# Kernel optimization log

Hardware: AMD Instinct MI355X
Metric: run time of the kernel (lower is better)

## Reference

```python
import jax, jax.numpy as jnp
import numpy as np

INPUT_DIM = 512
OUTPUT_DIM = 256
FAST_ITERATIONS = 100
BATCH = 65536


def setup_inputs() -> dict:
    key = jax.random.key(0)
    kx, kw, km = jax.random.split(key, 3)
    x = jax.random.normal(kx, (BATCH, INPUT_DIM), dtype=jnp.float32)
    # Xavier-uniform init for W [output_dim, input_dim]
    limit = np.sqrt(6.0 / (INPUT_DIM + OUTPUT_DIM))
    W = jax.random.uniform(kw, (OUTPUT_DIM, INPUT_DIM), dtype=jnp.float32,
                           minval=-limit, maxval=limit)
    # M is zeros in the module; use a small random M (spectral radius ~0.5)
    # so the 100-step recurrence is non-trivial but convergent.
    M = jax.random.normal(km, (OUTPUT_DIM, OUTPUT_DIM), dtype=jnp.float32) * (0.5 / np.sqrt(OUTPUT_DIM))
    return {"x": x, "W": W, "M": M}


def reference(x, W, M):
    Wx = x @ W.T  # [B, out]

    def step(y, _):
        return Wx - y @ M, None

    y, _ = jax.lax.scan(step, Wx, None, length=FAST_ITERATIONS)
    return y
```

## Files before the change

kernel.cpp:

```cpp
#include <hip/hip_runtime.h>
#include <hip/hip_bf16.h>


typedef float f32x4 __attribute__((ext_vector_type(4)));
typedef __bf16 bf16x8 __attribute__((ext_vector_type(8)));

#define IN 512
#define OUT 256
#define BATCH 65536

#define GLOAD_LDS16(gp, lp)                                                              \
    __builtin_amdgcn_global_load_lds((const __attribute__((address_space(1))) void*)(gp), \
                                     (__attribute__((address_space(3))) void*)(lp), 16, 0, 0)

__device__ __forceinline__ void chain_core(const float (*sA)[256], const float* __restrict__ B,
                                           int j, int q, float acc[8]) {
#pragma unroll
    for (int r = 0; r < 8; ++r) acc[r] = 0.f;
    const int kbase = q * 64;
#pragma unroll
    for (int it = 0; it < 16; ++it) {
        const int k = kbase + it * 4;
        const float b0 = B[(k + 0) * 256 + j];
        const float b1 = B[(k + 1) * 256 + j];
        const float b2 = B[(k + 2) * 256 + j];
        const float b3 = B[(k + 3) * 256 + j];
#pragma unroll
        for (int r = 0; r < 8; ++r) {
            const f32x4 av = *(const f32x4*)&sA[r][k];
            acc[r] += av[0] * b0 + av[1] * b1 + av[2] * b2 + av[3] * b3;
        }
    }
}

__global__ __launch_bounds__(1024) void nsm_chain_step(const float* __restrict__ Bmat,
                                                       const float* __restrict__ Pin,
                                                       float* __restrict__ Tout,
                                                       float* __restrict__ Pout,
                                                       const int first) {
    __shared__ float sA[8][256];
    __shared__ float ws[4][8][256];
    const int t = threadIdx.x, j = t & 255, q = t >> 8, b = blockIdx.x;
    float acc[8];
    const bool isT = (b < 32);
    if (isT) {
        const int i0 = b * 8;
        sA[2 * q][j]     = Bmat[(i0 + 2 * q) * 256 + j];
        sA[2 * q + 1][j] = Bmat[(i0 + 2 * q + 1) * 256 + j];
    } else {
        const int i0 = (b - 32) * 8;
        if (first) {
            sA[2 * q][j]     = Pin[j * IN + i0 + 2 * q];
            sA[2 * q + 1][j] = Pin[j * IN + i0 + 2 * q + 1];
        } else {
            sA[2 * q][j]     = Pin[(i0 + 2 * q) * 256 + j];
            sA[2 * q + 1][j] = Pin[(i0 + 2 * q + 1) * 256 + j];
        }
    }
    __syncthreads();
    chain_core(sA, Bmat, j, q, acc);
#pragma unroll
    for (int r = 0; r < 8; ++r) ws[q][r][j] = acc[r];
    __syncthreads();
#pragma unroll
    for (int d = 0; d < 2; ++d) {
        const int r = 2 * q + d;
        const float v = ws[0][r][j] + ws[1][r][j] + ws[2][r][j] + ws[3][r][j];
        if (isT) {
            const int i0 = b * 8;
            Tout[(i0 + r) * 256 + j] = v;
        } else {
            const int i0 = (b - 32) * 8;
            Pout[(i0 + r) * 256 + j] = first ? (sA[r][j] - v) : (sA[r][j] + v);
        }
    }
}

__global__ __launch_bounds__(1024) void nsm_chain_last(const float* __restrict__ Bmat,
                                                       const float* __restrict__ Pin,
                                                       __bf16* __restrict__ Ptk) {
    __shared__ float sA[8][256];
    __shared__ float ws[4][8][256];
    const int t = threadIdx.x, j = t & 255, q = t >> 8, b = blockIdx.x;
    const int i0 = b * 8;
    float acc[8];
    sA[2 * q][j]     = Pin[(i0 + 2 * q) * 256 + j];
    sA[2 * q + 1][j] = Pin[(i0 + 2 * q + 1) * 256 + j];
    __syncthreads();
    chain_core(sA, Bmat, j, q, acc);
#pragma unroll
    for (int r = 0; r < 8; ++r) ws[q][r][j] = acc[r];
    __syncthreads();
#pragma unroll
    for (int d = 0; d < 2; ++d) {
        const int r = 2 * q + d;
        const float v = ws[0][r][j] + ws[1][r][j] + ws[2][r][j] + ws[3][r][j];
        sA[r][j] += v;
    }
    __syncthreads();
    const int c = t >> 2, sub = t & 3;
    union { __bf16 h[2]; unsigned u; } pk;
    pk.h[0] = (__bf16)sA[sub * 2][c];
    pk.h[1] = (__bf16)sA[sub * 2 + 1][c];
    *(unsigned*)((void*)&Ptk[(size_t)(i0 >> 5) * 8192 + c * 32 + (i0 & 31) + sub * 2]) = pk.u;
}

__global__ __launch_bounds__(64, 2) void nsm_gemm_xP(const float* __restrict__ x,
                                                     const __bf16* __restrict__ Ptk,
                                                     float* __restrict__ y) {
    __shared__ float xs[2][64][32];
    const int lane = threadIdx.x;
    const int l15 = lane & 15, lhi = lane >> 4;

    const unsigned bid = blockIdx.x;
    const int xcd = bid & 7;
    const int w = bid >> 3;
    const int stripe = xcd * 128 + (w >> 1);
    const int nh = w & 1;
    const int m0 = stripe * 64;
    const int n0 = nh * 128;

    auto stageA = [&](int buf, int kt) {
        const int kk = kt * 32;
#pragma unroll
        for (int i = 0; i < 8; ++i) {
            const int r0 = i * 8;
            const int row = r0 + (lane >> 3);
            const int gch = (lane & 7) ^ (row & 7);
            GLOAD_LDS16(x + (size_t)(m0 + row) * IN + kk + gch * 4, &xs[buf][r0][0]);
        }
    };

    unsigned long long baddr = (unsigned long long)(const void*)Ptk +
                               (unsigned long long)(n0 * 64 + l15 * 64 + lhi * 16);
    bf16x8 b0[8], b1[8];

#define LOADB(SET)                                                                        \
    do {                                                                                  \
        const unsigned long long baddr2 = baddr + 4096;                                   \
        _Pragma("unroll")                                                                 \
        for (int nt = 0; nt < 8; ++nt)                                                    \
            asm volatile("global_load_dwordx4 %0, %1, off offset:%2"                      \
                         : "=v"(SET[nt])                                                  \
                         : "v"(nt < 4 ? baddr : baddr2), "n"((nt & 3) * 1024));           \
        baddr += 16384;                                                                   \
    } while (0)

    f32x4 acc[4][8];
#pragma unroll
    for (int a = 0; a < 4; ++a)
#pragma unroll
        for (int c = 0; c < 8; ++c) acc[a][c] = (f32x4){0.f, 0.f, 0.f, 0.f};

    stageA(0, 0);
    LOADB(b0);
    stageA(1, 1);
    LOADB(b1);

#pragma unroll
    for (int k = 0; k < 16; ++k) {
        if (k < 15) {
            asm volatile("s_waitcnt vmcnt(16)" ::: "memory");
        } else {
            asm volatile("s_waitcnt vmcnt(0)" ::: "memory");
        }
        __builtin_amdgcn_sched_barrier(0);

        const int buf = k & 1;
        f32x4 f0[4], f1[4];
#pragma unroll
        for (int mt = 0; mt < 4; ++mt) {
            const int row = mt * 16 + l15;
            const int c0 = (2 * lhi) ^ (row & 7);
            f0[mt] = *(const f32x4*)&xs[buf][row][c0 * 4];
            f1[mt] = *(const f32x4*)&xs[buf][row][(c0 ^ 1) * 4];
        }
        asm volatile("s_waitcnt lgkmcnt(0)" ::: "memory");
        __builtin_amdgcn_sched_barrier(0);
        if (k < 14) stageA(buf, k + 2);

        bf16x8 af[4];
#pragma unroll
        for (int mt = 0; mt < 4; ++mt) {
            bf16x8 t;
            t[0] = (__bf16)f0[mt][0]; t[1] = (__bf16)f0[mt][1];
            t[2] = (__bf16)f0[mt][2]; t[3] = (__bf16)f0[mt][3];
            t[4] = (__bf16)f1[mt][0]; t[5] = (__bf16)f1[mt][1];
            t[6] = (__bf16)f1[mt][2]; t[7] = (__bf16)f1[mt][3];
            af[mt] = t;
        }

        if ((k & 1) == 0) {
#pragma unroll
            for (int mt = 0; mt < 4; ++mt)
#pragma unroll
                for (int nt = 0; nt < 8; ++nt)
                    acc[mt][nt] = __builtin_amdgcn_mfma_f32_16x16x32_bf16(af[mt], b0[nt], acc[mt][nt], 0, 0, 0);
            if (k < 14) LOADB(b0);
        } else {
#pragma unroll
            for (int mt = 0; mt < 4; ++mt)
#pragma unroll
                for (int nt = 0; nt < 8; ++nt)
                    acc[mt][nt] = __builtin_amdgcn_mfma_f32_16x16x32_bf16(af[mt], b1[nt], acc[mt][nt], 0, 0, 0);
            if (k < 14) LOADB(b1);
        }
    }
#undef LOADB

#pragma unroll
    for (int mt = 0; mt < 4; ++mt) {
#pragma unroll
        for (int nt = 0; nt < 8; ++nt) {
            const int col = n0 + nt * 16 + l15;
            const int row = m0 + mt * 16 + lhi * 4;
#pragma unroll
            for (int r = 0; r < 4; ++r) y[(size_t)(row + r) * OUT + col] = acc[mt][nt][r];
        }
    }
}

extern "C" void kernel_launch(void* const* d_in, const int* in_sizes, int n_in,
                              void* d_out, int out_size, void* d_ws, size_t ws_size,
                              hipStream_t stream) {
    const float* x = (const float*)d_in[0];
    const float* W = (const float*)d_in[1];
    const float* M = (const float*)d_in[2];
    float* y = (float*)d_out;

    char* ws = (char*)d_ws;
    float* Ta = (float*)(ws);
    float* Tb = (float*)(ws + (256 << 10));
    float* Pa = (float*)(ws + (512 << 10));
    float* Pb = (float*)(ws + (1024 << 10));
    __bf16* Ptk = (__bf16*)(ws + (1536 << 10));

    nsm_chain_step<<<96, 1024, 0, stream>>>(M, W, Ta, Pa, 1);
    nsm_chain_step<<<96, 1024, 0, stream>>>(Ta, Pa, Tb, Pb, 0);
    nsm_chain_step<<<96, 1024, 0, stream>>>(Tb, Pb, Ta, Pa, 0);
    nsm_chain_last<<<64, 1024, 0, stream>>>(Ta, Pa, Ptk);
    nsm_gemm_xP<<<2048, 64, 0, stream>>>(x, Ptk, y);
}
```

Baseline: 66.68 us.

## Replicate bf16 P matrix across copies and stage output through LDS for vector stores

The small kernel that produces the transposed bf16 P matrix now writes it into eight replicas, and each GEMM block reads the replica chosen by its block index. This spreads the hot B-operand reads across different addresses to reduce contention at the shared L2/memory channels. The GEMM epilogue now writes accumulators into swizzled LDS and then emits 16-byte row-contiguous global stores in place of scattered 4-byte stores. The cost is eight times the write traffic in the producer kernel, extra workspace, and LDS round-trips in the epilogue that rely only on wave-level waitcnt ordering.

Result: slower. 69.26 us (+3.9%).

```diff
diff --git a/kernel.cpp b/kernel.cpp
--- a/kernel.cpp
+++ b/kernel.cpp
@@ -8,6 +8,8 @@
 #define IN 512
 #define OUT 256
 #define BATCH 65536
+#define NREP 8
+#define REP_ELEMS 131584
 
 #define GLOAD_LDS16(gp, lp)                                                              \
     __builtin_amdgcn_global_load_lds((const __attribute__((address_space(1))) void*)(gp), \
@@ -102,7 +104,10 @@
     union { __bf16 h[2]; unsigned u; } pk;
     pk.h[0] = (__bf16)sA[sub * 2][c];
     pk.h[1] = (__bf16)sA[sub * 2 + 1][c];
-    *(unsigned*)((void*)&Ptk[(size_t)(i0 >> 5) * 8192 + c * 32 + (i0 & 31) + sub * 2]) = pk.u;
+    const size_t idx = (size_t)(i0 >> 5) * 8192 + c * 32 + (i0 & 31) + sub * 2;
+#pragma unroll
+    for (int rep = 0; rep < NREP; ++rep)
+        *(unsigned*)((void*)&Ptk[(size_t)rep * REP_ELEMS + idx]) = pk.u;
 }
 
 __global__ __launch_bounds__(64, 2) void nsm_gemm_xP(const float* __restrict__ x,
@@ -117,6 +122,7 @@
     const int w = bid >> 3;
     const int stripe = xcd * 128 + (w >> 1);
     const int nh = w & 1;
+    const int rep = w & 7;
     const int m0 = stripe * 64;
     const int n0 = nh * 128;
 
@@ -131,7 +137,7 @@
         }
     };
 
-    unsigned long long baddr = (unsigned long long)(const void*)Ptk +
+    unsigned long long baddr = (unsigned long long)(const void*)(Ptk + (size_t)rep * REP_ELEMS) +
                                (unsigned long long)(n0 * 64 + l15 * 64 + lhi * 16);
     bf16x8 b0[8], b1[8];
 
@@ -208,15 +214,30 @@
     }
 #undef LOADB
 
+    float* eb = &xs[0][0][0];
 #pragma unroll
     for (int mt = 0; mt < 4; ++mt) {
 #pragma unroll
         for (int nt = 0; nt < 8; ++nt) {
-            const int col = n0 + nt * 16 + l15;
-            const int row = m0 + mt * 16 + lhi * 4;
-#pragma unroll
-            for (int r = 0; r < 4; ++r) y[(size_t)(row + r) * OUT + col] = acc[mt][nt][r];
-        }
+            const int col = nt * 16 + l15;
+            const int chunk = col >> 2;
+#pragma unroll
+            for (int r = 0; r < 4; ++r) {
+                const int row16 = lhi * 4 + r;
+                eb[row16 * 128 + ((chunk ^ (row16 & 7)) << 2) + (col & 3)] = acc[mt][nt][r];
+            }
+        }
+        asm volatile("s_waitcnt lgkmcnt(0)" ::: "memory");
+        __builtin_amdgcn_sched_barrier(0);
+#pragma unroll
+        for (int i = 0; i < 8; ++i) {
+            const int row16 = i * 2 + (lane >> 5);
+            const int g = lane & 31;
+            const f32x4 v = *(const f32x4*)&eb[row16 * 128 + ((g ^ (row16 & 7)) << 2)];
+            *(f32x4*)&y[(size_t)(m0 + mt * 16 + row16) * OUT + n0 + g * 4] = v;
+        }
+        asm volatile("s_waitcnt lgkmcnt(0)" ::: "memory");
+        __builtin_amdgcn_sched_barrier(0);
     }
 }
 
```
